# Optimization experiments

Measured on AMD Instinct MI355X. Metric: run time of the kernel, lower is better.

## Reference

```python
import jax, jax.numpy as jnp
import numpy as np

H, W = 250, 400
N_RAYS = H * W          # 100000 (one patch)
N_SAMPLES = 1_000_000
P, C, DIM = 50000, 16, 8
STEP_SIZE = 0.005
DENSITY_SHIFT = 0.0
DENSITY_SCALE = min(1.0 / (1.0 - DENSITY_SHIFT), 25.0)


def setup_inputs() -> dict:
    key = jax.random.key(0)
    ks = jax.random.split(key, 12)
    return {
        "trivecs": jax.random.normal(ks[0], (P, C, 3, DIM), dtype=jnp.float32),
        "densities": jax.random.normal(ks[1], (P, C), dtype=jnp.float32),
        "colors": jax.random.normal(ks[2], (P, C, 3), dtype=jnp.float32),
        "local_gweight_s": jax.random.uniform(ks[3], (N_SAMPLES, 3), dtype=jnp.float32),
        "local_gweight_l": jax.random.uniform(ks[4], (N_SAMPLES, 3), dtype=jnp.float32),
        "t_min": jax.random.uniform(ks[5], (N_RAYS,), dtype=jnp.float32),
        "bg": jax.random.uniform(ks[6], (3,), dtype=jnp.float32),
        "local_gindx_s": jax.random.randint(ks[7], (N_SAMPLES, 3), 0, DIM, dtype=jnp.int32),
        "local_gindx_l": jax.random.randint(ks[8], (N_SAMPLES, 3), 0, DIM, dtype=jnp.int32),
        "tensoRF_id": jax.random.randint(ks[9], (N_SAMPLES,), 0, P, dtype=jnp.int32),
        "ray_id": jnp.sort(jax.random.randint(ks[10], (N_SAMPLES,), 0, N_RAYS, dtype=jnp.int32)),
        "step_id": jax.random.randint(ks[11], (N_SAMPLES,), 0, 200, dtype=jnp.int32),
    }


def reference(trivecs, densities, colors, local_gweight_s, local_gweight_l,
              t_min, bg, local_gindx_s, local_gindx_l, tensoRF_id, ray_id, step_id):
    # --- compute_feature: trilinear tensor-decomposition gather ---
    def interp(a):
        vs = trivecs[tensoRF_id, :, a, local_gindx_s[:, a]]  # [N, C]
        vl = trivecs[tensoRF_id, :, a, local_gindx_l[:, a]]  # [N, C]
        return vs * local_gweight_s[:, a:a + 1] + vl * local_gweight_l[:, a:a + 1]

    feature = interp(0) * interp(1) * interp(2)               # [N, C]
    sigma = (feature * densities[tensoRF_id]).sum(axis=1)     # [N]
    color = jnp.einsum('nc,nck->nk', feature, colors[tensoRF_id])  # [N, 3]

    # --- density activation & alpha ---
    density = jax.nn.softplus(sigma - DENSITY_SHIFT * 10.0) * DENSITY_SCALE
    alpha = 1.0 - jnp.exp(-density * STEP_SIZE)               # [N]

    # --- Alphas2Weights: per-ray exclusive transmittance (ray_id sorted) ---
    log_t = -density * STEP_SIZE                              # == log(1 - alpha)
    seg_total = jax.ops.segment_sum(log_t, ray_id, num_segments=N_RAYS)  # [R]
    seg_offset = jnp.concatenate([jnp.zeros((1,), log_t.dtype),
                                  jnp.cumsum(seg_total)[:-1]])           # [R]
    excl = jnp.cumsum(log_t) - log_t - seg_offset[ray_id]     # within-segment excl cumsum
    weights = alpha * jnp.exp(excl)                           # [N]
    bg_weight = jnp.exp(seg_total)                            # [R], prod(1-alpha) per ray

    # --- ray compositing ---
    rgb = jax.nn.sigmoid(color)                               # [N, 3]
    rgb_map = jax.ops.segment_sum(weights[:, None] * rgb, ray_id, num_segments=N_RAYS)
    rgb_map = rgb_map + bg_weight[:, None] * bg[None, :]
    z_val = t_min[ray_id] + step_id.astype(jnp.float32) * STEP_SIZE
    depth_map = jax.ops.segment_sum(weights * z_val, ray_id, num_segments=N_RAYS)
    alpha_map = 1.0 - bg_weight

    rgb_map = rgb_map.T.reshape(3, H, W)
    depth_map = depth_map.reshape(H, W)
    alpha_map = alpha_map.reshape(H, W)
    return rgb_map, depth_map, alpha_map
```

## Files before the change

### kernel.cpp

```cpp
#include <hip/hip_runtime.h>
#include <math.h>

#define HN       250
#define WN       400
#define N_RAYS   (HN * WN)
#define N_SAMP   1000000
#define P_TENSO  50000
#define STEP_SZ  0.005f
#define DENS_SCALE 1.0f
#define NB_SCAN  ((P_TENSO + 1023) / 1024)


#define OFF_PACK    0
#define OFF_RESULTS 32000000
#define OFF_PERM    48000000
#define OFF_RT      52000000
#define OFF_CURSOR  56000000
#define OFF_STARTS  56200000
#define OFF_BSUMS   56400000
#define OFF_FLAG    56400512
#define OFF_RSTART  56401024
#define WS_NEED     (56401024 + 400004 + 64)

#define ROW_STRIDE 20
#define TV_F   (24 * ROW_STRIDE)
#define SLAB_F (TV_F + 16 + 48)

__global__ __launch_bounds__(256) void pack_bounds_rank(
    const int*   __restrict__ tenso_id,
    const int*   __restrict__ ray_id,
    const int*   __restrict__ gis, const int* __restrict__ gil,
    const float* __restrict__ gws, const float* __restrict__ gwl,
    int* __restrict__ cursor,
    int* __restrict__ rt,
    int* __restrict__ ray_start,
    float4* __restrict__ pack)
{
    int n = blockIdx.x * 256 + threadIdx.x;
    if (n >= N_SAMP) return;
    const int lane = threadIdx.x & 63;

    const int tid = tenso_id[n];
    const int rk = atomicAdd(&cursor[tid], 1);
    rt[n] = (tid << 16) | rk;

    unsigned bits = (unsigned)gis[n*3+0] | ((unsigned)gis[n*3+1] << 3) | ((unsigned)gis[n*3+2] << 6)
                  | ((unsigned)gil[n*3+0] << 9) | ((unsigned)gil[n*3+1] << 12) | ((unsigned)gil[n*3+2] << 15);
    float4 A = make_float4(gws[n*3+0], gws[n*3+1], gws[n*3+2], gwl[n*3+0]);
    float4 B = make_float4(gwl[n*3+1], gwl[n*3+2], __uint_as_float(bits), 0.0f);
    pack[(size_t)n * 2 + 0] = A;
    pack[(size_t)n * 2 + 1] = B;

    const int r = ray_id[n];
    const int rup = __shfl_up(r, 1);
    int rprev;
    if (lane == 0) rprev = (n == 0) ? -1 : ray_id[n - 1];
    else           rprev = rup;
    for (int q = rprev + 1; q <= r; ++q) ray_start[q] = n;
    if (n == N_SAMP - 1) {
        for (int q = r + 1; q <= N_RAYS; ++q) ray_start[q] = N_SAMP;
    }
}

__global__ __launch_bounds__(256) void scan_fused(
    const int* __restrict__ cursor,
    int* __restrict__ starts,
    int* __restrict__ bsums,
    int* __restrict__ flag)
{
    __shared__ int lds[257];
    const int b = blockIdx.x;
    const int t = threadIdx.x;
    const int base = b * 1024 + t * 4;

    int v[4]; int s = 0;
    #pragma unroll
    for (int i = 0; i < 4; ++i) {
        int idx = base + i;
        v[i] = (idx < P_TENSO) ? cursor[idx] : 0;
        s += v[i];
    }
    lds[t] = s;
    __syncthreads();
    for (int d = 1; d < 256; d <<= 1) {
        int x = (t >= d) ? lds[t - d] : 0;
        __syncthreads();
        lds[t] += x;
        __syncthreads();
    }
    if (t == 255) bsums[b] = lds[255];

    __threadfence();
    __syncthreads();
    if (t == 0) {
        atomicAdd(flag, 1);
        while (atomicAdd(flag, 0) < gridDim.x) { }
    }
    __syncthreads();
    __threadfence();

    if (t < 64) {
        int x = (t < b) ? bsums[t] : 0;
        #pragma unroll
        for (int m = 1; m < 64; m <<= 1) x += __shfl_xor(x, m);
        if (t == 0) lds[256] = x;
    }
    __syncthreads();
    const int pre = lds[256];

    int run = pre + ((t > 0) ? lds[t - 1] : 0);
    #pragma unroll
    for (int i = 0; i < 4; ++i) {
        int idx = base + i;
        if (idx < P_TENSO) starts[idx] = run;
        run += v[i];
    }
}

__global__ __launch_bounds__(256) void finalize_perm(
    const int* __restrict__ rt,
    const int* __restrict__ starts,
    int* __restrict__ perm)
{
    int n = blockIdx.x * 256 + threadIdx.x;
    if (n >= N_SAMP) return;
    const unsigned w = (unsigned)rt[n];
    int pos = starts[w >> 16] + (int)(w & 0xFFFFu);
    perm[pos] = n;
}

__global__ __launch_bounds__(128) void gather_phase(
    const float* __restrict__ trivecs,
    const float* __restrict__ densities,
    const float* __restrict__ colors,
    const int*   __restrict__ starts,
    const int*   __restrict__ counts,
    const int*   __restrict__ perm,
    const float4* __restrict__ pack,
    float* __restrict__ results_f)
{
    __shared__ __align__(16) float lds[2 * SLAB_F];
    const int lane = threadIdx.x & 63;
    const int wv   = threadIdx.x >> 6;
    const int t    = blockIdx.x * 2 + wv;
    if (t >= P_TENSO) return;

    const int start = starts[t];
    const int cnt   = counts[t];
    if (cnt == 0) return;

    float* slab = lds + wv * SLAB_F;
    float* dl   = slab + TV_F;
    float* cl   = dl + 16;

    const int pr = lane >> 1;
    const int h  = lane & 1;
    const int hc = h * 8;
    const int end = start + cnt;

    int p = start + pr;
    int n = perm[(p < end) ? p : (end - 1)];

    const float* tvg = trivecs + (size_t)t * 384;
    #pragma unroll
    for (int i = 0; i < 6; ++i) {
        int l = lane + i * 64;
        int c = l / 24;
        int rem = l - c * 24;
        slab[rem * ROW_STRIDE + c] = tvg[l];
    }
    if (lane < 16) dl[lane] = densities[(size_t)t * 16 + lane];
    if (lane < 48) {
        int c = lane / 3, k = lane - c * 3;
        cl[k * 16 + c] = colors[(size_t)t * 48 + lane];
    }

    const float4 dnA = *(const float4*)(dl + hc);
    const float4 dnB = *(const float4*)(dl + hc + 4);
    const float4 c0A = *(const float4*)(cl + hc);
    const float4 c0B = *(const float4*)(cl + hc + 4);
    const float4 c1A = *(const float4*)(cl + 16 + hc);
    const float4 c1B = *(const float4*)(cl + 16 + hc + 4);
    const float4 c2A = *(const float4*)(cl + 32 + hc);
    const float4 c2B = *(const float4*)(cl + 32 + hc + 4);

    const int niter = (cnt + 31) >> 5;

    for (int it = 0; it < niter; ++it) {
        const bool valid = (p < end);
        const int sn = n;

        const float4 A = pack[(size_t)sn * 2 + 0];
        const float4 B = pack[(size_t)sn * 2 + 1];

        if (it + 1 < niter) {
            p = start + (it + 1) * 32 + pr;
            n = perm[(p < end) ? p : (end - 1)];
        }

        const unsigned bits = __float_as_uint(B.z);

        float4 fA, fB;
        {
            const int is = bits & 7, il = (bits >> 9) & 7;
            const float4 vsA = *(const float4*)(slab + is * ROW_STRIDE + hc);
            const float4 vsB = *(const float4*)(slab + is * ROW_STRIDE + hc + 4);
            const float4 vlA = *(const float4*)(slab + il * ROW_STRIDE + hc);
            const float4 vlB = *(const float4*)(slab + il * ROW_STRIDE + hc + 4);
            fA.x = vsA.x * A.x + vlA.x * A.w;
            fA.y = vsA.y * A.x + vlA.y * A.w;
            fA.z = vsA.z * A.x + vlA.z * A.w;
            fA.w = vsA.w * A.x + vlA.w * A.w;
            fB.x = vsB.x * A.x + vlB.x * A.w;
            fB.y = vsB.y * A.x + vlB.y * A.w;
            fB.z = vsB.z * A.x + vlB.z * A.w;
            fB.w = vsB.w * A.x + vlB.w * A.w;
        }
        {
            const int is = (bits >> 3) & 7, il = (bits >> 12) & 7;
            const float4 vsA = *(const float4*)(slab + (8 + is) * ROW_STRIDE + hc);
            const float4 vsB = *(const float4*)(slab + (8 + is) * ROW_STRIDE + hc + 4);
            const float4 vlA = *(const float4*)(slab + (8 + il) * ROW_STRIDE + hc);
            const float4 vlB = *(const float4*)(slab + (8 + il) * ROW_STRIDE + hc + 4);
            fA.x *= vsA.x * A.y + vlA.x * B.x;
            fA.y *= vsA.y * A.y + vlA.y * B.x;
            fA.z *= vsA.z * A.y + vlA.z * B.x;
            fA.w *= vsA.w * A.y + vlA.w * B.x;
            fB.x *= vsB.x * A.y + vlB.x * B.x;
            fB.y *= vsB.y * A.y + vlB.y * B.x;
            fB.z *= vsB.z * A.y + vlB.z * B.x;
            fB.w *= vsB.w * A.y + vlB.w * B.x;
        }
        {
            const int is = (bits >> 6) & 7, il = (bits >> 15) & 7;
            const float4 vsA = *(const float4*)(slab + (16 + is) * ROW_STRIDE + hc);
            const float4 vsB = *(const float4*)(slab + (16 + is) * ROW_STRIDE + hc + 4);
            const float4 vlA = *(const float4*)(slab + (16 + il) * ROW_STRIDE + hc);
            const float4 vlB = *(const float4*)(slab + (16 + il) * ROW_STRIDE + hc + 4);
            fA.x *= vsA.x * A.z + vlA.x * B.y;
            fA.y *= vsA.y * A.z + vlA.y * B.y;
            fA.z *= vsA.z * A.z + vlA.z * B.y;
            fA.w *= vsA.w * A.z + vlA.w * B.y;
            fB.x *= vsB.x * A.z + vlB.x * B.y;
            fB.y *= vsB.y * A.z + vlB.y * B.y;
            fB.z *= vsB.z * A.z + vlB.z * B.y;
            fB.w *= vsB.w * A.z + vlB.w * B.y;
        }

        float s0 = fA.x*dnA.x + fA.y*dnA.y + fA.z*dnA.z + fA.w*dnA.w
                 + fB.x*dnB.x + fB.y*dnB.y + fB.z*dnB.z + fB.w*dnB.w;
        float s1 = fA.x*c0A.x + fA.y*c0A.y + fA.z*c0A.z + fA.w*c0A.w
                 + fB.x*c0B.x + fB.y*c0B.y + fB.z*c0B.z + fB.w*c0B.w;
        float s2 = fA.x*c1A.x + fA.y*c1A.y + fA.z*c1A.z + fA.w*c1A.w
                 + fB.x*c1B.x + fB.y*c1B.y + fB.z*c1B.z + fB.w*c1B.w;
        float s3 = fA.x*c2A.x + fA.y*c2A.y + fA.z*c2A.z + fA.w*c2A.w
                 + fB.x*c2B.x + fB.y*c2B.y + fB.z*c2B.z + fB.w*c2B.w;

        s0 += __shfl_xor(s0, 1);
        s1 += __shfl_xor(s1, 1);
        s2 += __shfl_xor(s2, 1);
        s3 += __shfl_xor(s3, 1);

        float2 val;
        if (h == 0) {
            float dens = fmaxf(s0, 0.0f) + __logf(1.0f + __expf(-fabsf(s0)));
            val.x = -(dens * DENS_SCALE) * STEP_SZ;
            val.y = 1.0f / (1.0f + __expf(-s1));
        } else {
            val.x = 1.0f / (1.0f + __expf(-s2));
            val.y = 1.0f / (1.0f + __expf(-s3));
        }
        if (valid) *(float2*)(results_f + (size_t)sn * 4 + 2 * h) = val;
    }
}

__global__ __launch_bounds__(256) void ray_render(
    const float4* __restrict__ results,
    const float*  __restrict__ t_min,
    const float*  __restrict__ bg,
    const int*    __restrict__ ray_start,
    const int*    __restrict__ step_id,
    float* __restrict__ out)
{
    const int lane = threadIdx.x & 63;
    const int g    = lane & 3;
    const int r    = (blockIdx.x * 256 + threadIdx.x) >> 2;
    if (r >= N_RAYS) return;
    const int s = ray_start[r];
    const int e = ray_start[r + 1];
    const float tmin_r = t_min[r];

    float eT = 1.0f, aR = 0.0f, aG = 0.0f, aB = 0.0f, aD = 0.0f;
    const int niter = (e - s + 3) >> 2;
    for (int it = 0; it < niter; ++it) {
        const int idx = s + it * 4 + g;
        const bool valid = (idx < e);
        const int ci = valid ? idx : (e - 1);
        const float4 res = results[ci];
        const float z = tmin_r + (float)step_id[ci] * STEP_SZ;
        const float elt = valid ? __expf(res.x) : 1.0f;

        float excl = 1.0f;
        const float v1 = __shfl_up(elt, 1, 4); if (g >= 1) excl *= v1;
        const float v2 = __shfl_up(elt, 2, 4); if (g >= 2) excl *= v2;
        const float v3 = __shfl_up(elt, 3, 4); if (g >= 3) excl *= v3;

        const float w = eT * excl * (1.0f - elt);
        aR += w * res.y;
        aG += w * res.z;
        aB += w * res.w;
        aD += w * z;

        const float tot = __shfl(excl * elt, 3, 4);
        eT *= tot;
    }

    aR += __shfl_xor(aR, 1); aR += __shfl_xor(aR, 2);
    aG += __shfl_xor(aG, 1); aG += __shfl_xor(aG, 2);
    aB += __shfl_xor(aB, 1); aB += __shfl_xor(aB, 2);
    aD += __shfl_xor(aD, 1); aD += __shfl_xor(aD, 2);

    const float outv = (g == 0) ? aR + eT * bg[0]
                     : (g == 1) ? aG + eT * bg[1]
                     : (g == 2) ? aB + eT * bg[2]
                     : aD;
    out[g * N_RAYS + r] = outv;
    if (g == 0) out[4 * N_RAYS + r] = 1.0f - eT;
}

__global__ __launch_bounds__(256) void trivec_render_fallback(
    const float* __restrict__ trivecs, const float* __restrict__ densities,
    const float* __restrict__ colors, const float* __restrict__ gws,
    const float* __restrict__ gwl, const float* __restrict__ t_min,
    const float* __restrict__ bg, const int* __restrict__ gis,
    const int* __restrict__ gil, const int* __restrict__ tenso_id,
    const int* __restrict__ ray_id, const int* __restrict__ step_id,
    float* __restrict__ out)
{
    const int lane = threadIdx.x & 63;
    const int r = blockIdx.x * 4 + (threadIdx.x >> 6);
    if (r >= N_RAYS) return;
    const int c = lane & 15;
    const int g = lane >> 4;
    int lo = 0, hi = N_SAMP;
    while (lo < hi) { int mid = (lo + hi) >> 1; if (ray_id[mid] < r) lo = mid + 1; else hi = mid; }
    const int seg_start = lo;
    hi = N_SAMP;
    while (lo < hi) { int mid = (lo + hi) >> 1; if (ray_id[mid] < r + 1) lo = mid + 1; else hi = mid; }
    const int seg_end = lo;
    const float tmin_r = t_min[r];
    float Tlog = 0.0f, accR = 0.0f, accG = 0.0f, accB = 0.0f, accD = 0.0f;
    const int niter = (seg_end - seg_start + 3) >> 2;
    for (int it = 0; it < niter; ++it) {
        const int n = seg_start + it * 4 + g;
        const bool valid = (n < seg_end);
        const int nc = valid ? n : (seg_end - 1);
        const int tid = tenso_id[nc];
        const float* tv = trivecs + (size_t)tid * 384 + c * 24;
        float f = 1.0f;
        #pragma unroll
        for (int a = 0; a < 3; ++a) {
            const int is = gis[nc*3+a], il = gil[nc*3+a];
            const float wS = gws[nc*3+a], wL = gwl[nc*3+a];
            f *= (tv[a*8+is] * wS + tv[a*8+il] * wL);
        }
        const float dns = densities[(size_t)tid * 16 + c];
        const float* colp = colors + ((size_t)tid * 16 + c) * 3;
        float s0 = f*dns, s1 = f*colp[0], s2 = f*colp[1], s3 = f*colp[2];
        #pragma unroll
        for (int m = 1; m < 16; m <<= 1) {
            s0 += __shfl_xor(s0, m); s1 += __shfl_xor(s1, m);
            s2 += __shfl_xor(s2, m); s3 += __shfl_xor(s3, m);
        }
        float dens = fmaxf(s0, 0.0f) + __logf(1.0f + __expf(-fabsf(s0)));
        const float lt = valid ? (-dens * STEP_SZ) : 0.0f;
        const float alpha = 1.0f - __expf(lt);
        const float rr = 1.0f/(1.0f+__expf(-s1)), gg = 1.0f/(1.0f+__expf(-s2)), bb = 1.0f/(1.0f+__expf(-s3));
        const float z = tmin_r + (float)step_id[nc] * STEP_SZ;
        const float lt0 = __shfl(lt,0), lt1 = __shfl(lt,16), lt2 = __shfl(lt,32), lt3 = __shfl(lt,48);
        float excl = Tlog;
        if (g > 0) excl += lt0;
        if (g > 1) excl += lt1;
        if (g > 2) excl += lt2;
        const float w = alpha * __expf(excl);
        Tlog += lt0 + lt1 + lt2 + lt3;
        accR += w*rr; accG += w*gg; accB += w*bb; accD += w*z;
    }
    accR += __shfl_xor(accR,16); accR += __shfl_xor(accR,32);
    accG += __shfl_xor(accG,16); accG += __shfl_xor(accG,32);
    accB += __shfl_xor(accB,16); accB += __shfl_xor(accB,32);
    accD += __shfl_xor(accD,16); accD += __shfl_xor(accD,32);
    const float bgw = __expf(Tlog);
    if (lane == 0) {
        out[0*N_RAYS+r] = accR + bgw*bg[0];
        out[1*N_RAYS+r] = accG + bgw*bg[1];
        out[2*N_RAYS+r] = accB + bgw*bg[2];
        out[3*N_RAYS+r] = accD;
        out[4*N_RAYS+r] = 1.0f - bgw;
    }
}

extern "C" void kernel_launch(void* const* d_in, const int* in_sizes, int n_in,
                              void* d_out, int out_size, void* d_ws, size_t ws_size,
                              hipStream_t stream) {
    const float* trivecs   = (const float*)d_in[0];
    const float* densities = (const float*)d_in[1];
    const float* colors    = (const float*)d_in[2];
    const float* gws       = (const float*)d_in[3];
    const float* gwl       = (const float*)d_in[4];
    const float* t_min     = (const float*)d_in[5];
    const float* bg        = (const float*)d_in[6];
    const int*   gis       = (const int*)d_in[7];
    const int*   gil       = (const int*)d_in[8];
    const int*   tenso_id  = (const int*)d_in[9];
    const int*   ray_id    = (const int*)d_in[10];
    const int*   step_id   = (const int*)d_in[11];
    float* out = (float*)d_out;

    if (ws_size < (size_t)WS_NEED) {
        trivec_render_fallback<<<(N_RAYS + 3) / 4, 256, 0, stream>>>(
            trivecs, densities, colors, gws, gwl, t_min, bg,
            gis, gil, tenso_id, ray_id, step_id, out);
        return;
    }

    char* ws = (char*)d_ws;
    float4* pack     = (float4*)(ws + OFF_PACK);
    float4* results  = (float4*)(ws + OFF_RESULTS);
    int*    perm     = (int*)(ws + OFF_PERM);
    int*    rt       = (int*)(ws + OFF_RT);
    int*    cursor   = (int*)(ws + OFF_CURSOR);
    int*    starts   = (int*)(ws + OFF_STARTS);
    int*    bsums    = (int*)(ws + OFF_BSUMS);
    int*    flag     = (int*)(ws + OFF_FLAG);
    int*    raystart = (int*)(ws + OFF_RSTART);

    hipMemsetAsync(ws + OFF_CURSOR, 0, (OFF_FLAG + 64) - OFF_CURSOR, stream);

    pack_bounds_rank<<<(N_SAMP + 255) / 256, 256, 0, stream>>>(
        tenso_id, ray_id, gis, gil, gws, gwl, cursor, rt, raystart, pack);
    scan_fused<<<NB_SCAN, 256, 0, stream>>>(cursor, starts, bsums, flag);
    finalize_perm<<<(N_SAMP + 255) / 256, 256, 0, stream>>>(
        rt, starts, perm);
    gather_phase<<<(P_TENSO + 1) / 2, 128, 0, stream>>>(
        trivecs, densities, colors, starts, cursor, perm, pack, (float*)results);
    ray_render<<<(N_RAYS * 4 + 255) / 256, 256, 0, stream>>>(
        results, t_min, bg, raystart, step_id, out);
}
```

Baseline: 275.0 us.

## Fuse preprocessing, scan and permutation into one persistent kernel with grid barriers

Merges the pack/rank, prefix-scan and permutation kernels into a single persistent kernel of 1536 blocks that grid-strides over samples. Spin-wait grid barriers on separate flag counters separate the three phases. This removes two kernel launches and their inter-kernel gaps. In exchange it adds global atomic barrier cost, and it depends on all blocks being co-resident, otherwise the barriers deadlock.

```diff
diff --git a/kernel.cpp b/kernel.cpp
--- a/kernel.cpp
+++ b/kernel.cpp
@@ -9,6 +9,7 @@
 #define STEP_SZ  0.005f
 #define DENS_SCALE 1.0f
 #define NB_SCAN  ((P_TENSO + 1023) / 1024)
+#define NB_PRE   1536
 
 
 #define OFF_PACK    0
@@ -26,7 +27,7 @@
 #define TV_F   (24 * ROW_STRIDE)
 #define SLAB_F (TV_F + 16 + 48)
 
-__global__ __launch_bounds__(256) void pack_bounds_rank(
+__global__ __launch_bounds__(256, 6) void fused_pre(
     const int*   __restrict__ tenso_id,
     const int*   __restrict__ ray_id,
     const int*   __restrict__ gis, const int* __restrict__ gil,
@@ -34,99 +35,108 @@
     int* __restrict__ cursor,
     int* __restrict__ rt,
     int* __restrict__ ray_start,
-    float4* __restrict__ pack)
-{
-    int n = blockIdx.x * 256 + threadIdx.x;
-    if (n >= N_SAMP) return;
-    const int lane = threadIdx.x & 63;
-
-    const int tid = tenso_id[n];
-    const int rk = atomicAdd(&cursor[tid], 1);
-    rt[n] = (tid << 16) | rk;
-
-    unsigned bits = (unsigned)gis[n*3+0] | ((unsigned)gis[n*3+1] << 3) | ((unsigned)gis[n*3+2] << 6)
-                  | ((unsigned)gil[n*3+0] << 9) | ((unsigned)gil[n*3+1] << 12) | ((unsigned)gil[n*3+2] << 15);
-    float4 A = make_float4(gws[n*3+0], gws[n*3+1], gws[n*3+2], gwl[n*3+0]);
-    float4 B = make_float4(gwl[n*3+1], gwl[n*3+2], __uint_as_float(bits), 0.0f);
-    pack[(size_t)n * 2 + 0] = A;
-    pack[(size_t)n * 2 + 1] = B;
-
-    const int r = ray_id[n];
-    const int rup = __shfl_up(r, 1);
-    int rprev;
-    if (lane == 0) rprev = (n == 0) ? -1 : ray_id[n - 1];
-    else           rprev = rup;
-    for (int q = rprev + 1; q <= r; ++q) ray_start[q] = n;
-    if (n == N_SAMP - 1) {
-        for (int q = r + 1; q <= N_RAYS; ++q) ray_start[q] = N_SAMP;
-    }
-}
-
-__global__ __launch_bounds__(256) void scan_fused(
-    const int* __restrict__ cursor,
+    float4* __restrict__ pack,
     int* __restrict__ starts,
     int* __restrict__ bsums,
-    int* __restrict__ flag)
+    int* __restrict__ flag,
+    int* __restrict__ perm)
 {
     __shared__ int lds[257];
     const int b = blockIdx.x;
     const int t = threadIdx.x;
-    const int base = b * 1024 + t * 4;
-
-    int v[4]; int s = 0;
-    #pragma unroll
-    for (int i = 0; i < 4; ++i) {
-        int idx = base + i;
-        v[i] = (idx < P_TENSO) ? cursor[idx] : 0;
-        s += v[i];
-    }
-    lds[t] = s;
-    __syncthreads();
-    for (int d = 1; d < 256; d <<= 1) {
-        int x = (t >= d) ? lds[t - d] : 0;
-        __syncthreads();
-        lds[t] += x;
-        __syncthreads();
-    }
-    if (t == 255) bsums[b] = lds[255];
+    const int lane = t & 63;
+
+    for (int n = b * 256 + t; n < N_SAMP; n += NB_PRE * 256) {
+        const int tid = tenso_id[n];
+        const int rk = atomicAdd(&cursor[tid], 1);
+        rt[n] = (tid << 16) | rk;
+
+        unsigned bits = (unsigned)gis[n*3+0] | ((unsigned)gis[n*3+1] << 3) | ((unsigned)gis[n*3+2] << 6)
+                      | ((unsigned)gil[n*3+0] << 9) | ((unsigned)gil[n*3+1] << 12) | ((unsigned)gil[n*3+2] << 15);
+        float4 A = make_float4(gws[n*3+0], gws[n*3+1], gws[n*3+2], gwl[n*3+0]);
+        float4 B = make_float4(gwl[n*3+1], gwl[n*3+2], __uint_as_float(bits), 0.0f);
+        pack[(size_t)n * 2 + 0] = A;
+        pack[(size_t)n * 2 + 1] = B;
+
+        const int r = ray_id[n];
+        const int rup = __shfl_up(r, 1);
+        int rprev;
+        if (lane == 0) rprev = (n == 0) ? -1 : ray_id[n - 1];
+        else           rprev = rup;
+        for (int q = rprev + 1; q <= r; ++q) ray_start[q] = n;
+        if (n == N_SAMP - 1) {
+            for (int q = r + 1; q <= N_RAYS; ++q) ray_start[q] = N_SAMP;
+        }
+    }
 
     __threadfence();
     __syncthreads();
     if (t == 0) {
-        atomicAdd(flag, 1);
-        while (atomicAdd(flag, 0) < gridDim.x) { }
+        atomicAdd(&flag[0], 1);
+        while (atomicAdd(&flag[0], 0) < NB_PRE) { }
     }
     __syncthreads();
     __threadfence();
 
-    if (t < 64) {
-        int x = (t < b) ? bsums[t] : 0;
+    if (b < NB_SCAN) {
+        const int base = b * 1024 + t * 4;
+        int v[4]; int s = 0;
         #pragma unroll
-        for (int m = 1; m < 64; m <<= 1) x += __shfl_xor(x, m);
-        if (t == 0) lds[256] = x;
-    }
+        for (int i = 0; i < 4; ++i) {
+            int idx = base + i;
+            v[i] = (idx < P_TENSO) ? cursor[idx] : 0;
+            s += v[i];
+        }
+        lds[t] = s;
+        __syncthreads();
+        for (int d = 1; d < 256; d <<= 1) {
+            int x = (t >= d) ? lds[t - d] : 0;
+            __syncthreads();
+            lds[t] += x;
+            __syncthreads();
+        }
+        if (t == 255) bsums[b] = lds[255];
+
+        __threadfence();
+        __syncthreads();
+        if (t == 0) {
+            atomicAdd(&flag[1], 1);
+            while (atomicAdd(&flag[1], 0) < NB_SCAN) { }
+        }
+        __syncthreads();
+        __threadfence();
+
+        if (t < 64) {
+            int x = (t < b) ? bsums[t] : 0;
+            #pragma unroll
+            for (int m = 1; m < 64; m <<= 1) x += __shfl_xor(x, m);
+            if (t == 0) lds[256] = x;
+        }
+        __syncthreads();
+        const int pre = lds[256];
+
+        int run = pre + ((t > 0) ? lds[t - 1] : 0);
+        #pragma unroll
+        for (int i = 0; i < 4; ++i) {
+            int idx = base + i;
+            if (idx < P_TENSO) starts[idx] = run;
+            run += v[i];
+        }
+    }
+
+    __threadfence();
     __syncthreads();
-    const int pre = lds[256];
-
-    int run = pre + ((t > 0) ? lds[t - 1] : 0);
-    #pragma unroll
-    for (int i = 0; i < 4; ++i) {
-        int idx = base + i;
-        if (idx < P_TENSO) starts[idx] = run;
-        run += v[i];
-    }
-}
-
-__global__ __launch_bounds__(256) void finalize_perm(
-    const int* __restrict__ rt,
-    const int* __restrict__ starts,
-    int* __restrict__ perm)
-{
-    int n = blockIdx.x * 256 + threadIdx.x;
-    if (n >= N_SAMP) return;
-    const unsigned w = (unsigned)rt[n];
-    int pos = starts[w >> 16] + (int)(w & 0xFFFFu);
-    perm[pos] = n;
+    if (t == 0) {
+        atomicAdd(&flag[2], 1);
+        while (atomicAdd(&flag[2], 0) < NB_PRE) { }
+    }
+    __syncthreads();
+    __threadfence();
+
+    for (int n = b * 256 + t; n < N_SAMP; n += NB_PRE * 256) {
+        const unsigned w = (unsigned)rt[n];
+        perm[starts[w >> 16] + (int)(w & 0xFFFFu)] = n;
+    }
 }
 
 __global__ __launch_bounds__(128) void gather_phase(
@@ -437,11 +447,9 @@
 
     hipMemsetAsync(ws + OFF_CURSOR, 0, (OFF_FLAG + 64) - OFF_CURSOR, stream);
 
-    pack_bounds_rank<<<(N_SAMP + 255) / 256, 256, 0, stream>>>(
-        tenso_id, ray_id, gis, gil, gws, gwl, cursor, rt, raystart, pack);
-    scan_fused<<<NB_SCAN, 256, 0, stream>>>(cursor, starts, bsums, flag);
-    finalize_perm<<<(N_SAMP + 255) / 256, 256, 0, stream>>>(
-        rt, starts, perm);
+    fused_pre<<<NB_PRE, 256, 0, stream>>>(
+        tenso_id, ray_id, gis, gil, gws, gwl,
+        cursor, rt, raystart, pack, starts, bsums, flag, perm);
     gather_phase<<<(P_TENSO + 1) / 2, 128, 0, stream>>>(
         trivecs, densities, colors, starts, cursor, perm, pack, (float*)results);
     ray_render<<<(N_RAYS * 4 + 255) / 256, 256, 0, stream>>>(
```

New measurement: 905.9 us. 3.29x slower.
